# Kernel optimization log

Hardware: AMD Instinct MI355X
Metric: run time of the kernel (lower is better)

The kernel has to match this reference:

```python
import jax, jax.numpy as jnp
import numpy as np

N_NODES = 50000
N_EDGES = 500000
IN_CH = 128
HID = 32
HEADS = 4
OUT_CH = 64
NEG_SLOPE = 0.2


def setup_inputs() -> dict:
    key = jax.random.key(0)
    ks = jax.random.split(key, 12)
    s = 0.1  # weight init scale
    x = jax.random.normal(ks[0], (N_NODES, IN_CH), jnp.float32)
    edge_index = jax.random.randint(ks[1], (2, N_EDGES), 0, N_NODES)
    # conv1: GATv2Conv(IN_CH, HID, heads=HEADS)
    W1l = jax.random.normal(ks[2], (IN_CH, HEADS * HID), jnp.float32) * s  # lin_l (source)
    W1r = jax.random.normal(ks[3], (IN_CH, HEADS * HID), jnp.float32) * s  # lin_r (target)
    att1 = jax.random.normal(ks[4], (HEADS, HID), jnp.float32) * s
    b1 = jnp.zeros((HEADS * HID,), jnp.float32)
    # conv2: GATv2Conv(HEADS*HID, OUT_CH, heads=1, concat=False)
    W2l = jax.random.normal(ks[5], (HEADS * HID, OUT_CH), jnp.float32) * s
    W2r = jax.random.normal(ks[6], (HEADS * HID, OUT_CH), jnp.float32) * s
    att2 = jax.random.normal(ks[7], (1, OUT_CH), jnp.float32) * s
    b2 = jnp.zeros((OUT_CH,), jnp.float32)
    return {"x": x, "edge_index": edge_index, "W1l": W1l, "W1r": W1r,
            "att1": att1, "b1": b1, "W2l": W2l, "W2r": W2r, "att2": att2, "b2": b2}


def gatv2_conv(x, src, dst, Wl, Wr, att, heads, ch, num_nodes):
    """GATv2Conv message passing. Returns [N, heads, ch] (pre-bias, pre-concat)."""
    xl = (x @ Wl).reshape(num_nodes, heads, ch)  # source transform
    xr = (x @ Wr).reshape(num_nodes, heads, ch)  # target transform
    xl_e = xl[src]                               # [E, H, C] gathered source feats
    m = jax.nn.leaky_relu(xl_e + xr[dst], NEG_SLOPE)
    score = jnp.einsum('ehc,hc->eh', m, att)     # [E, H]
    # segment softmax over incoming edges per destination node
    smax = jax.ops.segment_max(score, dst, num_segments=num_nodes)
    smax = jnp.where(jnp.isfinite(smax), smax, 0.0)
    p = jnp.exp(score - smax[dst])
    denom = jax.ops.segment_sum(p, dst, num_segments=num_nodes)
    alpha = p / (denom[dst] + 1e-16)
    out = jax.ops.segment_sum(alpha[:, :, None] * xl_e, dst, num_segments=num_nodes)
    return out


def reference(x, edge_index, W1l, W1r, att1, b1, W2l, W2r, att2, b2):
    n = x.shape[0]
    loop = jnp.arange(n, dtype=edge_index.dtype)
    src = jnp.concatenate([edge_index[0], loop])  # add self-loops (PyG default)
    dst = jnp.concatenate([edge_index[1], loop])
    # dropout(p=0.6) is identity in eval mode
    h = gatv2_conv(x, src, dst, W1l, W1r, att1, HEADS, HID, n)
    h = h.reshape(n, HEADS * HID) + b1            # concat=True
    h = jax.nn.elu(h)
    o = gatv2_conv(h, src, dst, W2l, W2r, att2, 1, OUT_CH, n)  # [N, 1, OUT]
    o = o + b2                                     # concat=False, heads=1 -> mean == identity
    return o[:, 0, :]
```

## Files before the change

### kernel.cpp

```cpp
#include <hip/hip_runtime.h>
#include <hip/hip_bf16.h>
#include <math.h>

#define N_NODESC 50000
#define N_EDGESC 500000
#define E_TOT    (N_EDGESC + N_NODESC)
#define IN_CH 128
#define HID 32
#define HEADS 4
#define HC (HEADS*HID)
#define OUT_CH 64
#define NEG_SLOPE 0.2f
#define NB_SCAN 196
#define N_STRIPS (N_NODESC/16)

typedef unsigned short u16;
typedef __attribute__((ext_vector_type(8))) short short8;
typedef __attribute__((ext_vector_type(8))) unsigned short ushort8v;
typedef __attribute__((ext_vector_type(4))) unsigned short ushort4v;
typedef __attribute__((ext_vector_type(4))) float floatx4;

__device__ __forceinline__ u16 f2bf(float f){
  unsigned u = __float_as_uint(f);
  return (u16)((u + 0x7FFFu + ((u >> 16) & 1u)) >> 16);
}
__device__ __forceinline__ float bf2f(u16 b){ return __uint_as_float(((unsigned)b) << 16); }
__device__ __forceinline__ float bflo(unsigned q){ return __uint_as_float(q << 16); }
__device__ __forceinline__ float bfhi(unsigned q){ return __uint_as_float(q & 0xFFFF0000u); }
__device__ __forceinline__ float lrelu(float v){ return fmaxf(v, NEG_SLOPE*v); }

__device__ __forceinline__ void edge_sd(const int* __restrict__ ei, int e, int& s, int& d){
  if (e < N_EDGESC){ s = ei[e]; d = ei[N_EDGESC + e]; }
  else { s = e - N_EDGESC; d = s; }
}

__global__ void k_misc(int* __restrict__ deg,
                       const float* __restrict__ X, u16* __restrict__ xhi, u16* __restrict__ xlo,
                       const float* __restrict__ W1l, const float* __restrict__ W1r,
                       const float* __restrict__ W2l, const float* __restrict__ W2r,
                       u16* __restrict__ w1lh, u16* __restrict__ w1rh,
                       u16* __restrict__ w2lh, u16* __restrict__ w2rh){
  int b = blockIdx.x;
  if (b < 196){
    int i = b*256 + threadIdx.x;
    if (i < N_NODESC) deg[i] = 0;
  } else if (b < 220){
    int bb = b - 196;
    const float* W; u16 *Th; int N, base;
    if (bb < 8)      { W=W1l; Th=w1lh; N=HC;     base=bb;    }
    else if (bb < 16){ W=W1r; Th=w1rh; N=HC;     base=bb-8;  }
    else if (bb < 20){ W=W2l; Th=w2lh; N=OUT_CH; base=bb-16; }
    else             { W=W2r; Th=w2rh; N=OUT_CH; base=bb-20; }
    int tid = base*256 + threadIdx.x;
    int lane = tid & 63;
    int t = (tid >> 6) & 3;
    int c = tid >> 8;
    int k0 = t*32 + (lane>>4)*8;
    int n  = c*16 + (lane&15);
    #pragma unroll
    for (int j=0;j<8;j++){
      Th[(size_t)tid*8 + j] = f2bf(W[(size_t)(k0+j)*N + n]);
    }
  } else {
    int i = (b-220)*256 + threadIdx.x;
    if (i < N_NODESC*HC/4){
      float4 v = ((const float4*)X)[i];
      ushort4 h, l;
      h.x = f2bf(v.x); l.x = f2bf(v.x - bf2f(h.x));
      h.y = f2bf(v.y); l.y = f2bf(v.y - bf2f(h.y));
      h.z = f2bf(v.z); l.z = f2bf(v.z - bf2f(h.z));
      h.w = f2bf(v.w); l.w = f2bf(v.w - bf2f(h.w));
      ((ushort4*)xhi)[i] = h;
      ((ushort4*)xlo)[i] = l;
    }
  }
}

__global__ void k_hist(const int* __restrict__ ei, int* __restrict__ deg){
  int e = blockIdx.x*blockDim.x + threadIdx.x;
  if (e >= E_TOT) return;
  int s, d; edge_sd(ei, e, s, d);
  atomicAdd(&deg[d], 1);
}

__global__ void k_scan_a(const int* __restrict__ deg, int* __restrict__ rs,
                         int* __restrict__ bsum){
  __shared__ int sh[256];
  int i = blockIdx.x*256 + threadIdx.x;
  int v = (i < N_NODESC) ? deg[i] : 0;
  sh[threadIdx.x] = v;
  __syncthreads();
  for (int off=1; off<256; off<<=1){
    int t = (threadIdx.x >= off) ? sh[threadIdx.x-off] : 0;
    __syncthreads();
    sh[threadIdx.x] += t;
    __syncthreads();
  }
  if (i < N_NODESC) rs[i] = sh[threadIdx.x] - v;
  if (threadIdx.x == 255) bsum[blockIdx.x] = sh[255];
}

__global__ void k_scan_b(int* __restrict__ bsum){
  __shared__ int sh[256];
  int v = (threadIdx.x < NB_SCAN) ? bsum[threadIdx.x] : 0;
  sh[threadIdx.x] = v;
  __syncthreads();
  for (int off=1; off<256; off<<=1){
    int t = (threadIdx.x >= off) ? sh[threadIdx.x-off] : 0;
    __syncthreads();
    sh[threadIdx.x] += t;
    __syncthreads();
  }
  if (threadIdx.x < NB_SCAN) bsum[threadIdx.x] = sh[threadIdx.x] - v;
}

__global__ void k_scan_c(int* __restrict__ rs, const int* __restrict__ bsum,
                         int* __restrict__ cursor){
  int i = blockIdx.x*256 + threadIdx.x;
  if (i >= N_NODESC) return;
  int v = rs[i] + bsum[blockIdx.x];
  rs[i] = v;
  cursor[i] = v;
}

__global__ void k_fill(const int* __restrict__ ei, int* __restrict__ cursor,
                       int* __restrict__ csrc){
  int e = blockIdx.x*blockDim.x + threadIdx.x;
  if (e >= E_TOT) return;
  int s, d; edge_sd(ei, e, s, d);
  int pos = atomicAdd(&cursor[d], 1);
  csrc[pos] = s;
}

template<int NCW, int SPB>
__launch_bounds__(256, 2)
__global__ void k_gemm_regB(const u16* __restrict__ Ahi, const u16* __restrict__ Alo,
                            const u16* __restrict__ BlT, const u16* __restrict__ BrT,
                            u16* __restrict__ Olb, u16* __restrict__ Orb){
  constexpr int NLD = 2*NCW*16;
  int wave = threadIdx.x >> 6, lane = threadIdx.x & 63;
  int m = lane & 15, quad = lane >> 4;
  bool isl = (wave < 2);
  int ctbase = (isl ? wave : wave - 2) * NCW;
  const u16* __restrict__ BT = isl ? BlT : BrT;
  u16* __restrict__ Ob = isl ? Olb : Orb;

  short8 breg[NCW][4];
  #pragma unroll
  for (int c=0;c<NCW;c++)
    #pragma unroll
    for (int t=0;t<4;t++)
      breg[c][t] = *(const short8*)(BT + ((size_t)(((ctbase+c)*4 + t)*64) + lane)*8);

  int strip0 = blockIdx.x * SPB;
  short8 ah[2][4], al[2][4];

  {
    const u16* p1 = Ahi + (size_t)(strip0*16 + m)*128 + quad*8;
    const u16* p2 = Alo + (size_t)(strip0*16 + m)*128 + quad*8;
    #pragma unroll
    for (int t=0;t<4;t++){
      ah[0][t] = *(const short8*)(p1 + t*32);
      al[0][t] = *(const short8*)(p2 + t*32);
    }
  }

  #pragma unroll
  for (int i=0;i<SPB;i++){
    int s = strip0 + i;
    if (s >= N_STRIPS) break;
    if (i+1 < SPB && s+1 < N_STRIPS){
      const u16* p1 = Ahi + (size_t)((s+1)*16 + m)*128 + quad*8;
      const u16* p2 = Alo + (size_t)((s+1)*16 + m)*128 + quad*8;
      #pragma unroll
      for (int t=0;t<4;t++){
        ah[(i+1)&1][t] = *(const short8*)(p1 + t*32);
        al[(i+1)&1][t] = *(const short8*)(p2 + t*32);
      }
    }
    const int b = i&1;
    floatx4 acc[NCW];
    #pragma unroll
    for (int c=0;c<NCW;c++) acc[c] = (floatx4){0.f,0.f,0.f,0.f};
    #pragma unroll
    for (int t=0;t<4;t++){
      #pragma unroll
      for (int c=0;c<NCW;c++){
        acc[c] = __builtin_amdgcn_mfma_f32_16x16x32_bf16(ah[b][t], breg[c][t], acc[c], 0,0,0);
        acc[c] = __builtin_amdgcn_mfma_f32_16x16x32_bf16(al[b][t], breg[c][t], acc[c], 0,0,0);
      }
    }
    int row0 = s*16;
    #pragma unroll
    for (int c=0;c<NCW;c++)
      #pragma unroll
      for (int r=0;r<4;r++)
        Ob[(size_t)(row0 + quad*4 + r)*NLD + (ctbase+c)*16 + m] = f2bf(acc[c][r]);
  }
}

__global__ void k_fused1(const int* __restrict__ rs, const int* __restrict__ deg,
                         const int* __restrict__ csrc, const u16* __restrict__ xlb,
                         const u16* __restrict__ xrb, const float* __restrict__ att,
                         const float* __restrict__ b1,
                         u16* __restrict__ Hhi, u16* __restrict__ Hlo, int d0){
  int wave = threadIdx.x >> 6;
  int lane = threadIdx.x & 63;
  int d = d0 + blockIdx.x*4 + wave;
  if (d >= N_NODESC) return;
  int g = lane >> 4;
  int l = lane & 15;

  float xrv[8], atv[8];
  {
    ushort8v xq = *(const ushort8v*)(xrb + (size_t)d*HC + 8*l);
    #pragma unroll
    for (int j=0;j<8;j++) xrv[j] = bf2f(xq[j]);
    float4 c = *(const float4*)(att + 8*l);
    float4 e = *(const float4*)(att + 8*l + 4);
    atv[0]=c.x; atv[1]=c.y; atv[2]=c.z; atv[3]=c.w;
    atv[4]=e.x; atv[5]=e.y; atv[6]=e.z; atv[7]=e.w;
  }

  int start = rs[d], degd = deg[d];

  float acc[8];
  #pragma unroll
  for (int j=0;j<8;j++) acc[j] = 0.f;
  float den = 0.f;

  int s_cur = csrc[start + ((g < degd) ? g : 0)];
  for (int i = 0; i < degd; i += 4){
    bool valid = (i + g < degd);
    int s = s_cur;
    int en = i + 4 + g;
    s_cur = csrc[start + ((en < degd) ? en : 0)];
    ushort8v q = *(const ushort8v*)(xlb + (size_t)s*HC + 8*l);
    float xv[8];
    float sc = 0.f;
    #pragma unroll
    for (int j=0;j<8;j++){
      xv[j] = bf2f(q[j]);
      sc = fmaf(lrelu(xv[j] + xrv[j]), atv[j], sc);
    }
    sc += __shfl_xor(sc, 1);
    sc += __shfl_xor(sc, 2);
    float p = valid ? __expf(sc) : 0.f;
    den += p;
    #pragma unroll
    for (int j=0;j<8;j++) acc[j] = fmaf(p, xv[j], acc[j]);
  }
  #pragma unroll
  for (int j=0;j<8;j++){
    acc[j] += __shfl_xor(acc[j], 16);
    acc[j] += __shfl_xor(acc[j], 32);
  }
  den += __shfl_xor(den, 16);
  den += __shfl_xor(den, 32);

  if (g == 0){
    float bv[8];
    float4 a = *(const float4*)(b1 + 8*l);
    float4 b = *(const float4*)(b1 + 8*l + 4);
    bv[0]=a.x; bv[1]=a.y; bv[2]=a.z; bv[3]=a.w;
    bv[4]=b.x; bv[5]=b.y; bv[6]=b.z; bv[7]=b.w;
    float inv = 1.f / (den + 1e-16f);
    u16 ohv[8], olv[8];
    #pragma unroll
    for (int j=0;j<8;j++){
      float o = acc[j]*inv + bv[j];
      o = (o > 0.f) ? o : (__expf(o) - 1.f);
      u16 h = f2bf(o);
      ohv[j] = h;
      olv[j] = f2bf(o - bf2f(h));
    }
    ushort4 h0 = {ohv[0],ohv[1],ohv[2],ohv[3]}, h1 = {ohv[4],ohv[5],ohv[6],ohv[7]};
    ushort4 l0 = {olv[0],olv[1],olv[2],olv[3]}, l1 = {olv[4],olv[5],olv[6],olv[7]};
    *(ushort4*)(Hhi + (size_t)d*HC + 8*l)     = h0;
    *(ushort4*)(Hhi + (size_t)d*HC + 8*l + 4) = h1;
    *(ushort4*)(Hlo + (size_t)d*HC + 8*l)     = l0;
    *(ushort4*)(Hlo + (size_t)d*HC + 8*l + 4) = l1;
  }
}

__global__ void k_fused2(const int* __restrict__ rs, const int* __restrict__ deg,
                         const int* __restrict__ csrc, const u16* __restrict__ xlb,
                         const u16* __restrict__ xrb, const float* __restrict__ att,
                         const float* __restrict__ b2, float* __restrict__ out){
  int wave = threadIdx.x >> 6;
  int lane = threadIdx.x & 63;
  int d = blockIdx.x*4 + wave;
  if (d >= N_NODESC) return;
  int g = lane >> 4;
  int l = lane & 15;

  float xrv[4], atv[4];
  {
    ushort4v xq = *(const ushort4v*)(xrb + (size_t)d*OUT_CH + 4*l);
    #pragma unroll
    for (int j=0;j<4;j++) xrv[j] = bf2f(xq[j]);
    float4 c = *(const float4*)(att + 4*l);
    atv[0]=c.x; atv[1]=c.y; atv[2]=c.z; atv[3]=c.w;
  }

  int start = rs[d], degd = deg[d];

  float acc[4] = {0.f,0.f,0.f,0.f};
  float den = 0.f;

  int s_cur = csrc[start + ((g < degd) ? g : 0)];
  for (int i = 0; i < degd; i += 4){
    bool valid = (i + g < degd);
    int s = s_cur;
    int en = i + 4 + g;
    s_cur = csrc[start + ((en < degd) ? en : 0)];
    uint2 q = *(const uint2*)(xlb + (size_t)s*OUT_CH + 4*l);
    float xv[4];
    xv[0]=bflo(q.x); xv[1]=bfhi(q.x);
    xv[2]=bflo(q.y); xv[3]=bfhi(q.y);
    float sc = 0.f;
    #pragma unroll
    for (int j=0;j<4;j++) sc = fmaf(lrelu(xv[j] + xrv[j]), atv[j], sc);
    sc += __shfl_xor(sc, 1);
    sc += __shfl_xor(sc, 2);
    sc += __shfl_xor(sc, 4);
    sc += __shfl_xor(sc, 8);
    float p = valid ? __expf(sc) : 0.f;
    den += p;
    #pragma unroll
    for (int j=0;j<4;j++) acc[j] = fmaf(p, xv[j], acc[j]);
  }
  #pragma unroll
  for (int j=0;j<4;j++){
    acc[j] += __shfl_xor(acc[j], 16);
    acc[j] += __shfl_xor(acc[j], 32);
  }
  den += __shfl_xor(den, 16);
  den += __shfl_xor(den, 32);

  if (g == 0){
    float4 bvv = *(const float4*)(b2 + 4*l);
    float inv = 1.f / (den + 1e-16f);
    float4 o;
    o.x = acc[0]*inv + bvv.x;
    o.y = acc[1]*inv + bvv.y;
    o.z = acc[2]*inv + bvv.z;
    o.w = acc[3]*inv + bvv.w;
    *(float4*)(out + (size_t)d*OUT_CH + 4*l) = o;
  }
}

extern "C" void kernel_launch(void* const* d_in, const int* in_sizes, int n_in,
                              void* d_out, int out_size, void* d_ws, size_t ws_size,
                              hipStream_t stream) {
  const float* x    = (const float*)d_in[0];
  const int*   ei   = (const int*)d_in[1];
  const float* W1l  = (const float*)d_in[2];
  const float* W1r  = (const float*)d_in[3];
  const float* att1 = (const float*)d_in[4];
  const float* b1   = (const float*)d_in[5];
  const float* W2l  = (const float*)d_in[6];
  const float* W2r  = (const float*)d_in[7];
  const float* att2 = (const float*)d_in[8];
  const float* b2   = (const float*)d_in[9];
  float* out = (float*)d_out;

  float* ws = (float*)d_ws;
  size_t off = 0;
  u16* xl1b = (u16*)(ws + off); off += (size_t)N_NODESC*HC/2;
  u16* xr1b = (u16*)(ws + off); off += (size_t)N_NODESC*HC/2;
  u16* xl2b = (u16*)(ws + off); off += (size_t)N_NODESC*OUT_CH/2;
  u16* xr2b = (u16*)(ws + off); off += (size_t)N_NODESC*OUT_CH/2;
  u16* xhi = (u16*)(ws + off); off += (size_t)N_NODESC*HC/2;
  u16* xlo = (u16*)(ws + off); off += (size_t)N_NODESC*HC/2;
  u16* hhi = (u16*)(ws + off); off += (size_t)N_NODESC*HC/2;
  u16* hlo = (u16*)(ws + off); off += (size_t)N_NODESC*HC/2;
  u16* w1lh = (u16*)(ws + off); off += IN_CH*HC/2;
  u16* w1rh = (u16*)(ws + off); off += IN_CH*HC/2;
  u16* w2lh = (u16*)(ws + off); off += HC*OUT_CH/2;
  u16* w2rh = (u16*)(ws + off); off += HC*OUT_CH/2;
  int* deg    = (int*)(ws + off); off += N_NODESC;
  int* rs     = (int*)(ws + off); off += N_NODESC;
  int* cursor = (int*)(ws + off); off += N_NODESC;
  int* bsum   = (int*)(ws + off); off += 256;
  int* csrc   = (int*)(ws + off); off += E_TOT;

  k_misc<<<220 + (N_NODESC*HC/4 + 255)/256, 256, 0, stream>>>(
      deg, x, xhi, xlo, W1l, W1r, W2l, W2r, w1lh, w1rh, w2lh, w2rh);
  k_hist<<<(E_TOT+255)/256, 256, 0, stream>>>(ei, deg);
  k_scan_a<<<NB_SCAN, 256, 0, stream>>>(deg, rs, bsum);
  k_scan_b<<<1, 256, 0, stream>>>(bsum);
  k_scan_c<<<NB_SCAN, 256, 0, stream>>>(rs, bsum, cursor);
  k_fill<<<(E_TOT+255)/256, 256, 0, stream>>>(ei, cursor, csrc);

  const int NB_G = (N_STRIPS + 3)/4;
  k_gemm_regB<4,4><<<NB_G, 256, 0, stream>>>(xhi, xlo, w1lh, w1rh, xl1b, xr1b);
  k_fused1<<<(N_NODESC/2+3)/4, 256, 0, stream>>>(rs, deg, csrc, xl1b, xr1b, att1, b1, hhi, hlo, 0);
  k_fused1<<<(N_NODESC/2+3)/4, 256, 0, stream>>>(rs, deg, csrc, xl1b, xr1b, att1, b1, hhi, hlo, N_NODESC/2);

  k_gemm_regB<2,4><<<NB_G, 256, 0, stream>>>(hhi, hlo, w2lh, w2rh, xl2b, xr2b);
  k_fused2<<<(N_NODESC+3)/4, 256, 0, stream>>>(rs, deg, csrc, xl2b, xr2b, att2, b2, out);
}
```

Baseline: 264.9 us.

## Merge histogram into prep kernel, fuse scan stages, widen layer-2 edge loop

Folds the degree histogram into the prep kernel, with degree zeroing moved to an async memset. The block-sum scan and add-back are merged into one kernel where every block rescans the 196 block sums. The two half-range k_fused1 launches become one launch. k_fused2 now uses 8 lanes per edge with 8 channels each, processing 8 edges per iteration with 16-byte loads, which cuts shuffle depth and raises edge-level parallelism. Together these reduce launch count and per-edge gather overhead, at the cost of redundant scan work per block.

```diff
diff --git a/kernel.cpp b/kernel.cpp
--- a/kernel.cpp
+++ b/kernel.cpp
@@ -13,11 +13,13 @@
 #define NEG_SLOPE 0.2f
 #define NB_SCAN 196
 #define N_STRIPS (N_NODESC/16)
+#define NB_HIST 2149
+#define NB_PREP 24
+#define NB_SPLIT 6250
 
 typedef unsigned short u16;
 typedef __attribute__((ext_vector_type(8))) short short8;
 typedef __attribute__((ext_vector_type(8))) unsigned short ushort8v;
-typedef __attribute__((ext_vector_type(4))) unsigned short ushort4v;
 typedef __attribute__((ext_vector_type(4))) float floatx4;
 
 __device__ __forceinline__ u16 f2bf(float f){
@@ -25,8 +27,6 @@
   return (u16)((u + 0x7FFFu + ((u >> 16) & 1u)) >> 16);
 }
 __device__ __forceinline__ float bf2f(u16 b){ return __uint_as_float(((unsigned)b) << 16); }
-__device__ __forceinline__ float bflo(unsigned q){ return __uint_as_float(q << 16); }
-__device__ __forceinline__ float bfhi(unsigned q){ return __uint_as_float(q & 0xFFFF0000u); }
 __device__ __forceinline__ float lrelu(float v){ return fmaxf(v, NEG_SLOPE*v); }
 
 __device__ __forceinline__ void edge_sd(const int* __restrict__ ei, int e, int& s, int& d){
@@ -34,18 +34,21 @@
   else { s = e - N_EDGESC; d = s; }
 }
 
-__global__ void k_misc(int* __restrict__ deg,
+__global__ void k_misc(const int* __restrict__ ei, int* __restrict__ deg,
                        const float* __restrict__ X, u16* __restrict__ xhi, u16* __restrict__ xlo,
                        const float* __restrict__ W1l, const float* __restrict__ W1r,
                        const float* __restrict__ W2l, const float* __restrict__ W2r,
                        u16* __restrict__ w1lh, u16* __restrict__ w1rh,
                        u16* __restrict__ w2lh, u16* __restrict__ w2rh){
   int b = blockIdx.x;
-  if (b < 196){
-    int i = b*256 + threadIdx.x;
-    if (i < N_NODESC) deg[i] = 0;
-  } else if (b < 220){
-    int bb = b - 196;
+  if (b < NB_HIST){
+    int e = b*256 + threadIdx.x;
+    if (e < E_TOT){
+      int s, d; edge_sd(ei, e, s, d);
+      atomicAdd(&deg[d], 1);
+    }
+  } else if (b < NB_HIST + NB_PREP){
+    int bb = b - NB_HIST;
     const float* W; u16 *Th; int N, base;
     if (bb < 8)      { W=W1l; Th=w1lh; N=HC;     base=bb;    }
     else if (bb < 16){ W=W1r; Th=w1rh; N=HC;     base=bb-8;  }
@@ -62,7 +65,7 @@
       Th[(size_t)tid*8 + j] = f2bf(W[(size_t)(k0+j)*N + n]);
     }
   } else {
-    int i = (b-220)*256 + threadIdx.x;
+    int i = (b - NB_HIST - NB_PREP)*256 + threadIdx.x;
     if (i < N_NODESC*HC/4){
       float4 v = ((const float4*)X)[i];
       ushort4 h, l;
@@ -74,13 +77,6 @@
       ((ushort4*)xlo)[i] = l;
     }
   }
-}
-
-__global__ void k_hist(const int* __restrict__ ei, int* __restrict__ deg){
-  int e = blockIdx.x*blockDim.x + threadIdx.x;
-  if (e >= E_TOT) return;
-  int s, d; edge_sd(ei, e, s, d);
-  atomicAdd(&deg[d], 1);
 }
 
 __global__ void k_scan_a(const int* __restrict__ deg, int* __restrict__ rs,
@@ -100,7 +96,8 @@
   if (threadIdx.x == 255) bsum[blockIdx.x] = sh[255];
 }
 
-__global__ void k_scan_b(int* __restrict__ bsum){
+__global__ void k_scan_bc(int* __restrict__ rs, const int* __restrict__ bsum,
+                          int* __restrict__ cursor){
   __shared__ int sh[256];
   int v = (threadIdx.x < NB_SCAN) ? bsum[threadIdx.x] : 0;
   sh[threadIdx.x] = v;
@@ -111,16 +108,13 @@
     sh[threadIdx.x] += t;
     __syncthreads();
   }
-  if (threadIdx.x < NB_SCAN) bsum[threadIdx.x] = sh[threadIdx.x] - v;
-}
-
-__global__ void k_scan_c(int* __restrict__ rs, const int* __restrict__ bsum,
-                         int* __restrict__ cursor){
+  int add = sh[blockIdx.x] - bsum[blockIdx.x];
   int i = blockIdx.x*256 + threadIdx.x;
-  if (i >= N_NODESC) return;
-  int v = rs[i] + bsum[blockIdx.x];
-  rs[i] = v;
-  cursor[i] = v;
+  if (i < N_NODESC){
+    int v2 = rs[i] + add;
+    rs[i] = v2;
+    cursor[i] = v2;
+  }
 }
 
 __global__ void k_fill(const int* __restrict__ ei, int* __restrict__ cursor,
@@ -203,10 +197,10 @@
                          const int* __restrict__ csrc, const u16* __restrict__ xlb,
                          const u16* __restrict__ xrb, const float* __restrict__ att,
                          const float* __restrict__ b1,
-                         u16* __restrict__ Hhi, u16* __restrict__ Hlo, int d0){
+                         u16* __restrict__ Hhi, u16* __restrict__ Hlo){
   int wave = threadIdx.x >> 6;
   int lane = threadIdx.x & 63;
-  int d = d0 + blockIdx.x*4 + wave;
+  int d = blockIdx.x*4 + wave;
   if (d >= N_NODESC) return;
   int g = lane >> 4;
   int l = lane & 15;
@@ -291,62 +285,73 @@
   int lane = threadIdx.x & 63;
   int d = blockIdx.x*4 + wave;
   if (d >= N_NODESC) return;
-  int g = lane >> 4;
-  int l = lane & 15;
-
-  float xrv[4], atv[4];
+  int g = lane >> 3;
+  int l = lane & 7;
+
+  float xrv[8], atv[8];
   {
-    ushort4v xq = *(const ushort4v*)(xrb + (size_t)d*OUT_CH + 4*l);
-    #pragma unroll
-    for (int j=0;j<4;j++) xrv[j] = bf2f(xq[j]);
-    float4 c = *(const float4*)(att + 4*l);
+    ushort8v xq = *(const ushort8v*)(xrb + (size_t)d*OUT_CH + 8*l);
+    #pragma unroll
+    for (int j=0;j<8;j++) xrv[j] = bf2f(xq[j]);
+    float4 c = *(const float4*)(att + 8*l);
+    float4 e = *(const float4*)(att + 8*l + 4);
     atv[0]=c.x; atv[1]=c.y; atv[2]=c.z; atv[3]=c.w;
+    atv[4]=e.x; atv[5]=e.y; atv[6]=e.z; atv[7]=e.w;
   }
 
   int start = rs[d], degd = deg[d];
 
-  float acc[4] = {0.f,0.f,0.f,0.f};
+  float acc[8];
+  #pragma unroll
+  for (int j=0;j<8;j++) acc[j] = 0.f;
   float den = 0.f;
 
   int s_cur = csrc[start + ((g < degd) ? g : 0)];
-  for (int i = 0; i < degd; i += 4){
+  for (int i = 0; i < degd; i += 8){
     bool valid = (i + g < degd);
     int s = s_cur;
-    int en = i + 4 + g;
+    int en = i + 8 + g;
     s_cur = csrc[start + ((en < degd) ? en : 0)];
-    uint2 q = *(const uint2*)(xlb + (size_t)s*OUT_CH + 4*l);
-    float xv[4];
-    xv[0]=bflo(q.x); xv[1]=bfhi(q.x);
-    xv[2]=bflo(q.y); xv[3]=bfhi(q.y);
+    ushort8v q = *(const ushort8v*)(xlb + (size_t)s*OUT_CH + 8*l);
+    float xv[8];
     float sc = 0.f;
     #pragma unroll
-    for (int j=0;j<4;j++) sc = fmaf(lrelu(xv[j] + xrv[j]), atv[j], sc);
+    for (int j=0;j<8;j++){
+      xv[j] = bf2f(q[j]);
+      sc = fmaf(lrelu(xv[j] + xrv[j]), atv[j], sc);
+    }
     sc += __shfl_xor(sc, 1);
     sc += __shfl_xor(sc, 2);
     sc += __shfl_xor(sc, 4);
-    sc += __shfl_xor(sc, 8);
     float p = valid ? __expf(sc) : 0.f;
     den += p;
     #pragma unroll
-    for (int j=0;j<4;j++) acc[j] = fmaf(p, xv[j], acc[j]);
-  }
-  #pragma unroll
-  for (int j=0;j<4;j++){
+    for (int j=0;j<8;j++) acc[j] = fmaf(p, xv[j], acc[j]);
+  }
+  #pragma unroll
+  for (int j=0;j<8;j++){
+    acc[j] += __shfl_xor(acc[j], 8);
     acc[j] += __shfl_xor(acc[j], 16);
     acc[j] += __shfl_xor(acc[j], 32);
   }
+  den += __shfl_xor(den, 8);
   den += __shfl_xor(den, 16);
   den += __shfl_xor(den, 32);
 
   if (g == 0){
-    float4 bvv = *(const float4*)(b2 + 4*l);
+    float bv[8];
+    float4 a = *(const float4*)(b2 + 8*l);
+    float4 b = *(const float4*)(b2 + 8*l + 4);
+    bv[0]=a.x; bv[1]=a.y; bv[2]=a.z; bv[3]=a.w;
+    bv[4]=b.x; bv[5]=b.y; bv[6]=b.z; bv[7]=b.w;
     float inv = 1.f / (den + 1e-16f);
-    float4 o;
-    o.x = acc[0]*inv + bvv.x;
-    o.y = acc[1]*inv + bvv.y;
-    o.z = acc[2]*inv + bvv.z;
-    o.w = acc[3]*inv + bvv.w;
-    *(float4*)(out + (size_t)d*OUT_CH + 4*l) = o;
+    float4 o0, o1;
+    o0.x = acc[0]*inv + bv[0]; o0.y = acc[1]*inv + bv[1];
+    o0.z = acc[2]*inv + bv[2]; o0.w = acc[3]*inv + bv[3];
+    o1.x = acc[4]*inv + bv[4]; o1.y = acc[5]*inv + bv[5];
+    o1.z = acc[6]*inv + bv[6]; o1.w = acc[7]*inv + bv[7];
+    *(float4*)(out + (size_t)d*OUT_CH + 8*l)     = o0;
+    *(float4*)(out + (size_t)d*OUT_CH + 8*l + 4) = o1;
   }
 }
 
@@ -385,18 +390,16 @@
   int* bsum   = (int*)(ws + off); off += 256;
   int* csrc   = (int*)(ws + off); off += E_TOT;
 
-  k_misc<<<220 + (N_NODESC*HC/4 + 255)/256, 256, 0, stream>>>(
-      deg, x, xhi, xlo, W1l, W1r, W2l, W2r, w1lh, w1rh, w2lh, w2rh);
-  k_hist<<<(E_TOT+255)/256, 256, 0, stream>>>(ei, deg);
+  hipMemsetAsync(deg, 0, N_NODESC*sizeof(int), stream);
+  k_misc<<<NB_HIST + NB_PREP + NB_SPLIT, 256, 0, stream>>>(
+      ei, deg, x, xhi, xlo, W1l, W1r, W2l, W2r, w1lh, w1rh, w2lh, w2rh);
   k_scan_a<<<NB_SCAN, 256, 0, stream>>>(deg, rs, bsum);
-  k_scan_b<<<1, 256, 0, stream>>>(bsum);
-  k_scan_c<<<NB_SCAN, 256, 0, stream>>>(rs, bsum, cursor);
+  k_scan_bc<<<NB_SCAN, 256, 0, stream>>>(rs, bsum, cursor);
   k_fill<<<(E_TOT+255)/256, 256, 0, stream>>>(ei, cursor, csrc);
 
   const int NB_G = (N_STRIPS + 3)/4;
   k_gemm_regB<4,4><<<NB_G, 256, 0, stream>>>(xhi, xlo, w1lh, w1rh, xl1b, xr1b);
-  k_fused1<<<(N_NODESC/2+3)/4, 256, 0, stream>>>(rs, deg, csrc, xl1b, xr1b, att1, b1, hhi, hlo, 0);
-  k_fused1<<<(N_NODESC/2+3)/4, 256, 0, stream>>>(rs, deg, csrc, xl1b, xr1b, att1, b1, hhi, hlo, N_NODESC/2);
+  k_fused1<<<(N_NODESC+3)/4, 256, 0, stream>>>(rs, deg, csrc, xl1b, xr1b, att1, b1, hhi, hlo);
 
   k_gemm_regB<2,4><<<NB_G, 256, 0, stream>>>(hhi, hlo, w2lh, w2rh, xl2b, xr2b);
   k_fused2<<<(N_NODESC+3)/4, 256, 0, stream>>>(rs, deg, csrc, xl2b, xr2b, att2, b2, out);
```

Measured after the change: 250.1 us. 5.6% less time.
